# Kernel optimization log

Measured on AMD Instinct MI355X. Metric: run time of the kernel, lower is better.

The kernel has to match this reference:

```python
import jax, jax.numpy as jnp
import numpy as np

P_DROP = 0.2  # matches nn.Dropout(0.2) in the module __init__ (forward's dropout_p arg is unused)
DROPOUT_KEY = jax.random.key(42)  # deterministic dropout mask for reproducible baseline


def setup_inputs() -> dict:
    key = jax.random.key(0)
    kq, kk, kv = jax.random.split(key, 3)
    B, Sq, Sk, D, Dv = 4, 4096, 4096, 64, 64
    return {
        "q": jax.random.normal(kq, (B, Sq, D), dtype=jnp.float32),
        "k": jax.random.normal(kk, (B, Sk, D), dtype=jnp.float32),
        "v": jax.random.normal(kv, (B, Sk, Dv), dtype=jnp.float32),
        "scale_factor": 1,
        "dropout_p": 0,
    }


def reference(q, k, v, scale_factor, dropout_p):
    # qk = q @ k^T, scaled  -> [B, Sq, Sk] (full attention matrix, as in the original)
    qk = jnp.einsum("bqd,bkd->bqk", q, k) * scale_factor
    probs = jax.nn.softmax(qk, axis=-1)
    # dropout (train-mode nn.Dropout(p=0.2)): deterministic mask, inverted scaling
    keep = jax.random.bernoulli(DROPOUT_KEY, 1.0 - P_DROP, probs.shape)
    probs = jnp.where(keep, probs / (1.0 - P_DROP), 0.0)
    # output = probs @ v -> [B, Sq, Dv]
    return jnp.einsum("bqk,bkd->bqd", probs, v)
```

## Files before the change

kernel.cpp:

```cpp
#include <hip/hip_runtime.h>
#include <hip/hip_bf16.h>
#include <stdint.h>

typedef __attribute__((ext_vector_type(8))) _Float16 f16x8;
typedef __attribute__((ext_vector_type(4))) float f32x4;

static constexpr int BATCH = 4;
static constexpr int SEQ = 4096;
static constexpr int DIM = 64;
static constexpr int QB = 128;
static constexpr int NQB = SEQ / QB;
static constexpr uint32_t KEEP_THRESH = 0xCCCCCE00u;
static constexpr float LOG2E = 1.44269504088896340736f;

static constexpr size_t PB_BYTES = (QB * 64 + QB * 2) * 4;
static __host__ __device__ constexpr size_t ws_need(int ns) {
  return (size_t)BATCH * NQB * ns * PB_BYTES;
}
static __host__ __device__ constexpr size_t onum_bytes(int ns) {
  return (size_t)BATCH * NQB * ns * QB * 64 * 4;
}

__device__ __forceinline__ int lds_swz(int row, int colbyte) {
  return row * 128 + (colbyte ^ ((row & 7) << 4));
}

#define ROTL(x, r) (__builtin_amdgcn_alignbit((x), (x), 32 - (r)))

__device__ __forceinline__ bool tf_keep(uint32_t j42) {
  const uint32_t k1 = 42u;
  const uint32_t k2 = 0x1BD11BDAu ^ k1;
  uint32_t x1 = j42;
  uint32_t x0 = x1;
  x1 = ROTL(x1, 13) ^ x0;
  x0 += x1; x1 = ROTL(x1, 15) ^ x0;
  x0 += x1; x1 = ROTL(x1, 26) ^ x0;
  x0 += x1; x1 = ROTL(x1, 6)  ^ x0;
  x0 += k1;      x1 += k2 + 1u;
  x0 += x1; x1 = ROTL(x1, 17) ^ x0;
  x0 += x1; x1 = ROTL(x1, 29) ^ x0;
  x0 += x1; x1 = ROTL(x1, 16) ^ x0;
  x0 += x1; x1 = ROTL(x1, 24) ^ x0;
  x0 += k2;      x1 += 2u;
  x0 += x1; x1 = ROTL(x1, 13) ^ x0;
  x0 += x1; x1 = ROTL(x1, 15) ^ x0;
  x0 += x1; x1 = ROTL(x1, 26) ^ x0;
  x0 += x1; x1 = ROTL(x1, 6)  ^ x0;
    x1 += k1 + 3u;
  x0 += x1; x1 = ROTL(x1, 17) ^ x0;
  x0 += x1; x1 = ROTL(x1, 29) ^ x0;
  x0 += x1; x1 = ROTL(x1, 16) ^ x0;
  x0 += x1; x1 = ROTL(x1, 24) ^ x0;
  x0 += k1;      x1 += k2 + 4u;
  x0 += x1; x1 = ROTL(x1, 13) ^ x0;
  x0 += x1; x1 = ROTL(x1, 15) ^ x0;
  x0 += x1; x1 = ROTL(x1, 26) ^ x0;
  x0 += x1; x1 = ROTL(x1, 6)  ^ x0;
  x0 += k2;      x1 += 5u;
  return (x0 ^ x1) < KEEP_THRESH;
}

__device__ __forceinline__ float fexp2(float x) {
  float r;
  asm("v_exp_f32 %0, %1" : "=v"(r) : "v"(x));
  return r;
}

template<int CTRL>
__device__ __forceinline__ float dpp_movf(float x) {
  return __int_as_float(
      __builtin_amdgcn_mov_dpp(__float_as_int(x), CTRL, 0xF, 0xF, true));
}
__device__ __forceinline__ float red16_max(float v) {
  v = fmaxf(v, dpp_movf<0xB1>(v));
  v = fmaxf(v, dpp_movf<0x4E>(v));
  v = fmaxf(v, dpp_movf<0x141>(v));
  v = fmaxf(v, dpp_movf<0x140>(v));
  return v;
}
__device__ __forceinline__ float red16_add(float v) {
  v += dpp_movf<0xB1>(v);
  v += dpp_movf<0x4E>(v);
  v += dpp_movf<0x141>(v);
  v += dpp_movf<0x140>(v);
  return v;
}

template<bool PARTIAL, int NS>
__global__ __launch_bounds__(256, 3) void attn_kernel(
    const float* __restrict__ Q, const float* __restrict__ K, const float* __restrict__ V,
    const uint32_t* __restrict__ scale_raw,
    float* __restrict__ Out, float* __restrict__ onum, float* __restrict__ ml)
{
  __shared__ __align__(16) _Float16 Kld[64 * 64];
  __shared__ __align__(16) _Float16 Vt[64 * 64];
  __shared__ __align__(16) _Float16 Pld[4][32 * 64];

  const int b   = blockIdx.y;
  const int q0  = blockIdx.x * QB;
  const int tid = threadIdx.x;
  const int w    = tid >> 6;
  const int lane = tid & 63;
  const int l15  = lane & 15;
  const int l4   = lane >> 4;

  float scale;
  {
    uint32_t sb = *scale_raw;
    int e = (int)((sb >> 23) & 0xFFu);
    if (sb == 0u) scale = 0.0f;
    else if (e == 0 || e == 255) scale = (float)(int)sb;
    else scale = __uint_as_float(sb);
  }
  const float qscale = scale * LOG2E;

  const int qw = q0 + w * 32;

  uint32_t rcb42[2][4];
#pragma unroll
  for (int m = 0; m < 2; ++m)
#pragma unroll
    for (int r = 0; r < 4; ++r)
      rcb42[m][r] = ((uint32_t)(b * SEQ + qw + 16 * m + 4 * l4 + r)) * (uint32_t)SEQ + 42u;

  f16x8 aq[2][2];
#pragma unroll
  for (int m = 0; m < 2; ++m)
#pragma unroll
    for (int c = 0; c < 2; ++c) {
      const float* qp = Q + ((size_t)(b * SEQ + qw + 16 * m + l15)) * DIM + l4 * 8 + 32 * c;
      f16x8 h;
#pragma unroll
      for (int j = 0; j < 8; ++j) h[j] = (_Float16)(qp[j] * qscale);
      aq[m][c] = h;
    }

  float m_r[2][4], l_p[2][4];
  f32x4 Oacc[2][4];
#pragma unroll
  for (int m = 0; m < 2; ++m)
#pragma unroll
    for (int r = 0; r < 4; ++r) { m_r[m][r] = -INFINITY; l_p[m][r] = 0.0f; }
#pragma unroll
  for (int m = 0; m < 2; ++m)
#pragma unroll
    for (int n = 0; n < 4; ++n) Oacc[m][n] = f32x4{0.f, 0.f, 0.f, 0.f};

  const int nt = PARTIAL ? (SEQ / 64) / NS : SEQ / 64;
  const int t0 = PARTIAL ? (int)blockIdx.z * nt : 0;

  const int kr  = tid >> 4;
  const int kd0 = (tid & 15) * 4;
  const int vd  = tid & 63;
  const int vq  = tid >> 6;

  for (int kt = 0; kt < nt; ++kt) {
    const int kbase = (t0 + kt) * 64;
    __syncthreads();
#pragma unroll
    for (int i = 0; i < 4; ++i) {
      int k = kr + 16 * i;
      float4 kf = *(const float4*)(K + ((size_t)(b * SEQ + kbase + k)) * DIM + kd0);
      _Float16 h0 = (_Float16)kf.x, h1 = (_Float16)kf.y,
               h2 = (_Float16)kf.z, h3 = (_Float16)kf.w;
      *(ushort4*)((char*)Kld + lds_swz(k, kd0 * 2)) = ushort4{
        __builtin_bit_cast(unsigned short, h0), __builtin_bit_cast(unsigned short, h1),
        __builtin_bit_cast(unsigned short, h2), __builtin_bit_cast(unsigned short, h3)};
    }
#pragma unroll
    for (int i = 0; i < 4; ++i) {
      int k0 = vq * 4 + 16 * i;
      const float* vp = V + ((size_t)(b * SEQ + kbase + k0)) * DIM + vd;
      float v0 = vp[0], v1 = vp[DIM], v2 = vp[2 * DIM], v3 = vp[3 * DIM];
      unsigned int p01 = __builtin_bit_cast(unsigned int, __builtin_amdgcn_cvt_pkrtz(v0, v1));
      unsigned int p23 = __builtin_bit_cast(unsigned int, __builtin_amdgcn_cvt_pkrtz(v2, v3));
      *(uint2*)((char*)Vt + lds_swz(vd, k0 * 2)) = uint2{p01, p23};
    }
    __syncthreads();

    char* pw = (char*)&Pld[w][0];

#pragma unroll
    for (int m = 0; m < 2; ++m) {
      f32x4 s[4];
#pragma unroll
      for (int n = 0; n < 4; ++n) {
        f32x4 acc = f32x4{0.f, 0.f, 0.f, 0.f};
#pragma unroll
        for (int c = 0; c < 2; ++c) {
          int off = lds_swz(16 * n + l15, (l4 * 8 + 32 * c) * 2);
          f16x8 bk = *(const f16x8*)((char*)Kld + off);
          acc = __builtin_amdgcn_mfma_f32_16x16x32_f16(aq[m][c], bk, acc, 0, 0, 0);
        }
        s[n] = acc;
      }

      float mnew[4];
#pragma unroll
      for (int r = 0; r < 4; ++r)
        mnew[r] = red16_max(fmaxf(fmaxf(s[0][r], s[1][r]), fmaxf(s[2][r], s[3][r])));

#pragma unroll
      for (int r = 0; r < 4; ++r) {
        float mn = fmaxf(m_r[m][r], mnew[r]);
        float corr = fexp2(m_r[m][r] - mn);
        m_r[m][r] = mn;
        l_p[m][r] *= corr;
#pragma unroll
        for (int n = 0; n < 4; ++n) Oacc[m][n][r] *= corr;
      }

#pragma unroll
      for (int n = 0; n < 4; ++n) {
        uint32_t cb = (uint32_t)(kbase + l15 + 16 * n);
#pragma unroll
        for (int r = 0; r < 4; ++r) {
          float e = fexp2(s[n][r] - m_r[m][r]);
          l_p[m][r] += e;
          float p = tf_keep(rcb42[m][r] + cb) ? e : 0.0f;
          *(_Float16*)(pw + lds_swz(16 * m + 4 * l4 + r, (l15 + 16 * n) * 2)) = (_Float16)p;
        }
      }
    }

    asm volatile("s_waitcnt lgkmcnt(0)" ::: "memory");
    __builtin_amdgcn_sched_barrier(0);

    f16x8 pa[2][2];
#pragma unroll
    for (int m = 0; m < 2; ++m)
#pragma unroll
      for (int c = 0; c < 2; ++c)
        pa[m][c] = *(const f16x8*)(pw + lds_swz(16 * m + l15, (l4 * 8 + 32 * c) * 2));
#pragma unroll
    for (int n = 0; n < 4; ++n) {
#pragma unroll
      for (int c = 0; c < 2; ++c) {
        f16x8 bv = *(const f16x8*)((char*)Vt + lds_swz(l15 + 16 * n, (l4 * 8 + 32 * c) * 2));
#pragma unroll
        for (int m = 0; m < 2; ++m)
          Oacc[m][n] = __builtin_amdgcn_mfma_f32_16x16x32_f16(pa[m][c], bv, Oacc[m][n], 0, 0, 0);
      }
    }
  }

  if (PARTIAL) {
    const int pb = ((b * NQB + (int)blockIdx.x) * NS + (int)blockIdx.z);
    float* op = onum + (size_t)pb * (QB * 64);
#pragma unroll
    for (int m = 0; m < 2; ++m)
#pragma unroll
      for (int r = 0; r < 4; ++r) {
        int row = w * 32 + 16 * m + 4 * l4 + r;
        float lr = red16_add(l_p[m][r]);
#pragma unroll
        for (int n = 0; n < 4; ++n)
          op[row * 64 + l15 + 16 * n] = Oacc[m][n][r];
        if (l15 == 0) {
          ml[(size_t)pb * (QB * 2) + row * 2 + 0] = m_r[m][r];
          ml[(size_t)pb * (QB * 2) + row * 2 + 1] = lr;
        }
      }
  } else {
#pragma unroll
    for (int m = 0; m < 2; ++m)
#pragma unroll
      for (int r = 0; r < 4; ++r) {
        float L = red16_add(l_p[m][r]);
        float inv = 1.0f / (L * 0.8f);
        int qg = qw + 16 * m + 4 * l4 + r;
        float* op = Out + ((size_t)(b * SEQ + qg)) * DIM + l15;
#pragma unroll
        for (int n = 0; n < 4; ++n)
          op[16 * n] = Oacc[m][n][r] * inv;
      }
  }
}

template<int NS>
__global__ __launch_bounds__(256) void combine_kernel(
    const float* __restrict__ onum, const float* __restrict__ ml, float* __restrict__ Out)
{
  const int w = threadIdx.x >> 6;
  const int lane = threadIdx.x & 63;
  const int rid = blockIdx.x * 4 + w;
  const int b = rid >> 12;
  const int qrow = rid & 4095;
  const int qb = qrow >> 7;
  const int r128 = qrow & 127;
  const int pb0 = (b * NQB + qb) * NS;

  float m[NS], l[NS];
  float M = -INFINITY;
#pragma unroll
  for (int s = 0; s < NS; ++s) {
    m[s] = ml[(size_t)(pb0 + s) * (QB * 2) + r128 * 2 + 0];
    l[s] = ml[(size_t)(pb0 + s) * (QB * 2) + r128 * 2 + 1];
    M = fmaxf(M, m[s]);
  }
  float L = 0.0f, acc = 0.0f;
#pragma unroll
  for (int s = 0; s < NS; ++s) {
    float sc = fexp2(m[s] - M);
    L += l[s] * sc;
    acc += onum[(size_t)(pb0 + s) * (QB * 64) + r128 * 64 + lane] * sc;
  }
  Out[(size_t)rid * 64 + lane] = acc / (L * 0.8f);
}

extern "C" void kernel_launch(void* const* d_in, const int* in_sizes, int n_in,
                              void* d_out, int out_size, void* d_ws, size_t ws_size,
                              hipStream_t stream) {
  const float* Q = (const float*)d_in[0];
  const float* K = (const float*)d_in[1];
  const float* V = (const float*)d_in[2];
  const uint32_t* scale_raw = (const uint32_t*)d_in[3];
  float* Out = (float*)d_out;

  if (ws_size >= ws_need(8)) {
    float* onum = (float*)d_ws;
    float* ml = (float*)((char*)d_ws + onum_bytes(8));
    attn_kernel<true, 8><<<dim3(NQB, BATCH, 8), 256, 0, stream>>>(
        Q, K, V, scale_raw, nullptr, onum, ml);
    combine_kernel<8><<<SEQ * BATCH / 4, 256, 0, stream>>>(onum, ml, Out);
  } else if (ws_size >= ws_need(4)) {
    float* onum = (float*)d_ws;
    float* ml = (float*)((char*)d_ws + onum_bytes(4));
    attn_kernel<true, 4><<<dim3(NQB, BATCH, 4), 256, 0, stream>>>(
        Q, K, V, scale_raw, nullptr, onum, ml);
    combine_kernel<4><<<SEQ * BATCH / 4, 256, 0, stream>>>(onum, ml, Out);
  } else {
    attn_kernel<false, 1><<<dim3(NQB, BATCH, 1), 256, 0, stream>>>(
        Q, K, V, scale_raw, Out, nullptr, nullptr);
  }
}
```

Baseline: 172.3 us.

## Shrink query block to 64 rows with one 16-row MFMA tile per wave

Halves the query block from 128 to 64 rows so each wave handles 16 query rows instead of 32, removing the inner m loop and cutting per-wave register state. This doubles the grid size, which improves parallelism and load balance. In exchange, K/V tiles are loaded and converted twice as often per query row, roughly doubling global-to-LDS traffic, and launch bounds occupancy hint drops from 3 to 2.

```diff
diff --git a/kernel.cpp b/kernel.cpp
--- a/kernel.cpp
+++ b/kernel.cpp
@@ -8,7 +8,7 @@
 static constexpr int BATCH = 4;
 static constexpr int SEQ = 4096;
 static constexpr int DIM = 64;
-static constexpr int QB = 128;
+static constexpr int QB = 64;
 static constexpr int NQB = SEQ / QB;
 static constexpr uint32_t KEEP_THRESH = 0xCCCCCE00u;
 static constexpr float LOG2E = 1.44269504088896340736f;
@@ -87,14 +87,14 @@
 }
 
 template<bool PARTIAL, int NS>
-__global__ __launch_bounds__(256, 3) void attn_kernel(
+__global__ __launch_bounds__(256, 2) void attn_kernel(
     const float* __restrict__ Q, const float* __restrict__ K, const float* __restrict__ V,
     const uint32_t* __restrict__ scale_raw,
     float* __restrict__ Out, float* __restrict__ onum, float* __restrict__ ml)
 {
   __shared__ __align__(16) _Float16 Kld[64 * 64];
   __shared__ __align__(16) _Float16 Vt[64 * 64];
-  __shared__ __align__(16) _Float16 Pld[4][32 * 64];
+  __shared__ __align__(16) _Float16 Pld[4][16 * 64];
 
   const int b   = blockIdx.y;
   const int q0  = blockIdx.x * QB;
@@ -114,37 +114,29 @@
   }
   const float qscale = scale * LOG2E;
 
-  const int qw = q0 + w * 32;
-
-  uint32_t rcb42[2][4];
-#pragma unroll
-  for (int m = 0; m < 2; ++m)
-#pragma unroll
-    for (int r = 0; r < 4; ++r)
-      rcb42[m][r] = ((uint32_t)(b * SEQ + qw + 16 * m + 4 * l4 + r)) * (uint32_t)SEQ + 42u;
-
-  f16x8 aq[2][2];
-#pragma unroll
-  for (int m = 0; m < 2; ++m)
-#pragma unroll
-    for (int c = 0; c < 2; ++c) {
-      const float* qp = Q + ((size_t)(b * SEQ + qw + 16 * m + l15)) * DIM + l4 * 8 + 32 * c;
-      f16x8 h;
-#pragma unroll
-      for (int j = 0; j < 8; ++j) h[j] = (_Float16)(qp[j] * qscale);
-      aq[m][c] = h;
-    }
-
-  float m_r[2][4], l_p[2][4];
-  f32x4 Oacc[2][4];
-#pragma unroll
-  for (int m = 0; m < 2; ++m)
-#pragma unroll
-    for (int r = 0; r < 4; ++r) { m_r[m][r] = -INFINITY; l_p[m][r] = 0.0f; }
-#pragma unroll
-  for (int m = 0; m < 2; ++m)
-#pragma unroll
-    for (int n = 0; n < 4; ++n) Oacc[m][n] = f32x4{0.f, 0.f, 0.f, 0.f};
+  const int qw = q0 + w * 16;
+
+  uint32_t rcb42[4];
+#pragma unroll
+  for (int r = 0; r < 4; ++r)
+    rcb42[r] = ((uint32_t)(b * SEQ + qw + 4 * l4 + r)) * (uint32_t)SEQ + 42u;
+
+  f16x8 aq[2];
+#pragma unroll
+  for (int c = 0; c < 2; ++c) {
+    const float* qp = Q + ((size_t)(b * SEQ + qw + l15)) * DIM + l4 * 8 + 32 * c;
+    f16x8 h;
+#pragma unroll
+    for (int j = 0; j < 8; ++j) h[j] = (_Float16)(qp[j] * qscale);
+    aq[c] = h;
+  }
+
+  float m_r[4], l_p[4];
+  f32x4 Oacc[4];
+#pragma unroll
+  for (int r = 0; r < 4; ++r) { m_r[r] = -INFINITY; l_p[r] = 0.0f; }
+#pragma unroll
+  for (int n = 0; n < 4; ++n) Oacc[n] = f32x4{0.f, 0.f, 0.f, 0.f};
 
   const int nt = PARTIAL ? (SEQ / 64) / NS : SEQ / 64;
   const int t0 = PARTIAL ? (int)blockIdx.z * nt : 0;
@@ -178,68 +170,60 @@
     }
     __syncthreads();
 
+    f32x4 s[4];
+#pragma unroll
+    for (int n = 0; n < 4; ++n) {
+      f32x4 acc = f32x4{0.f, 0.f, 0.f, 0.f};
+#pragma unroll
+      for (int c = 0; c < 2; ++c) {
+        int off = lds_swz(16 * n + l15, (l4 * 8 + 32 * c) * 2);
+        f16x8 bk = *(const f16x8*)((char*)Kld + off);
+        acc = __builtin_amdgcn_mfma_f32_16x16x32_f16(aq[c], bk, acc, 0, 0, 0);
+      }
+      s[n] = acc;
+    }
+
+    float mnew[4];
+#pragma unroll
+    for (int r = 0; r < 4; ++r)
+      mnew[r] = red16_max(fmaxf(fmaxf(s[0][r], s[1][r]), fmaxf(s[2][r], s[3][r])));
+
+#pragma unroll
+    for (int r = 0; r < 4; ++r) {
+      float mn = fmaxf(m_r[r], mnew[r]);
+      float corr = fexp2(m_r[r] - mn);
+      m_r[r] = mn;
+      l_p[r] *= corr;
+#pragma unroll
+      for (int n = 0; n < 4; ++n) Oacc[n][r] *= corr;
+    }
+
     char* pw = (char*)&Pld[w][0];
-
-#pragma unroll
-    for (int m = 0; m < 2; ++m) {
-      f32x4 s[4];
-#pragma unroll
-      for (int n = 0; n < 4; ++n) {
-        f32x4 acc = f32x4{0.f, 0.f, 0.f, 0.f};
-#pragma unroll
-        for (int c = 0; c < 2; ++c) {
-          int off = lds_swz(16 * n + l15, (l4 * 8 + 32 * c) * 2);
-          f16x8 bk = *(const f16x8*)((char*)Kld + off);
-          acc = __builtin_amdgcn_mfma_f32_16x16x32_f16(aq[m][c], bk, acc, 0, 0, 0);
-        }
-        s[n] = acc;
-      }
-
-      float mnew[4];
-#pragma unroll
-      for (int r = 0; r < 4; ++r)
-        mnew[r] = red16_max(fmaxf(fmaxf(s[0][r], s[1][r]), fmaxf(s[2][r], s[3][r])));
-
+#pragma unroll
+    for (int n = 0; n < 4; ++n) {
+      uint32_t cb = (uint32_t)(kbase + l15 + 16 * n);
 #pragma unroll
       for (int r = 0; r < 4; ++r) {
-        float mn = fmaxf(m_r[m][r], mnew[r]);
-        float corr = fexp2(m_r[m][r] - mn);
-        m_r[m][r] = mn;
-        l_p[m][r] *= corr;
-#pragma unroll
-        for (int n = 0; n < 4; ++n) Oacc[m][n][r] *= corr;
-      }
-
-#pragma unroll
-      for (int n = 0; n < 4; ++n) {
-        uint32_t cb = (uint32_t)(kbase + l15 + 16 * n);
-#pragma unroll
-        for (int r = 0; r < 4; ++r) {
-          float e = fexp2(s[n][r] - m_r[m][r]);
-          l_p[m][r] += e;
-          float p = tf_keep(rcb42[m][r] + cb) ? e : 0.0f;
-          *(_Float16*)(pw + lds_swz(16 * m + 4 * l4 + r, (l15 + 16 * n) * 2)) = (_Float16)p;
-        }
+        float e = fexp2(s[n][r] - m_r[r]);
+        l_p[r] += e;
+        float p = tf_keep(rcb42[r] + cb) ? e : 0.0f;
+        *(_Float16*)(pw + lds_swz(4 * l4 + r, (l15 + 16 * n) * 2)) = (_Float16)p;
       }
     }
 
     asm volatile("s_waitcnt lgkmcnt(0)" ::: "memory");
     __builtin_amdgcn_sched_barrier(0);
 
-    f16x8 pa[2][2];
-#pragma unroll
-    for (int m = 0; m < 2; ++m)
-#pragma unroll
-      for (int c = 0; c < 2; ++c)
-        pa[m][c] = *(const f16x8*)(pw + lds_swz(16 * m + l15, (l4 * 8 + 32 * c) * 2));
+    f16x8 pa[2];
+#pragma unroll
+    for (int c = 0; c < 2; ++c)
+      pa[c] = *(const f16x8*)(pw + lds_swz(l15, (l4 * 8 + 32 * c) * 2));
 #pragma unroll
     for (int n = 0; n < 4; ++n) {
 #pragma unroll
       for (int c = 0; c < 2; ++c) {
         f16x8 bv = *(const f16x8*)((char*)Vt + lds_swz(l15 + 16 * n, (l4 * 8 + 32 * c) * 2));
-#pragma unroll
-        for (int m = 0; m < 2; ++m)
-          Oacc[m][n] = __builtin_amdgcn_mfma_f32_16x16x32_f16(pa[m][c], bv, Oacc[m][n], 0, 0, 0);
+        Oacc[n] = __builtin_amdgcn_mfma_f32_16x16x32_f16(pa[c], bv, Oacc[n], 0, 0, 0);
       }
     }
   }
@@ -248,32 +232,28 @@
     const int pb = ((b * NQB + (int)blockIdx.x) * NS + (int)blockIdx.z);
     float* op = onum + (size_t)pb * (QB * 64);
 #pragma unroll
-    for (int m = 0; m < 2; ++m)
-#pragma unroll
-      for (int r = 0; r < 4; ++r) {
-        int row = w * 32 + 16 * m + 4 * l4 + r;
-        float lr = red16_add(l_p[m][r]);
-#pragma unroll
-        for (int n = 0; n < 4; ++n)
-          op[row * 64 + l15 + 16 * n] = Oacc[m][n][r];
-        if (l15 == 0) {
-          ml[(size_t)pb * (QB * 2) + row * 2 + 0] = m_r[m][r];
-          ml[(size_t)pb * (QB * 2) + row * 2 + 1] = lr;
-        }
+    for (int r = 0; r < 4; ++r) {
+      int row = w * 16 + 4 * l4 + r;
+      float lr = red16_add(l_p[r]);
+#pragma unroll
+      for (int n = 0; n < 4; ++n)
+        op[row * 64 + l15 + 16 * n] = Oacc[n][r];
+      if (l15 == 0) {
+        ml[(size_t)pb * (QB * 2) + row * 2 + 0] = m_r[r];
+        ml[(size_t)pb * (QB * 2) + row * 2 + 1] = lr;
       }
+    }
   } else {
 #pragma unroll
-    for (int m = 0; m < 2; ++m)
-#pragma unroll
-      for (int r = 0; r < 4; ++r) {
-        float L = red16_add(l_p[m][r]);
-        float inv = 1.0f / (L * 0.8f);
-        int qg = qw + 16 * m + 4 * l4 + r;
-        float* op = Out + ((size_t)(b * SEQ + qg)) * DIM + l15;
-#pragma unroll
-        for (int n = 0; n < 4; ++n)
-          op[16 * n] = Oacc[m][n][r] * inv;
-      }
+    for (int r = 0; r < 4; ++r) {
+      float L = red16_add(l_p[r]);
+      float inv = 1.0f / (L * 0.8f);
+      int qg = qw + 4 * l4 + r;
+      float* op = Out + ((size_t)(b * SEQ + qg)) * DIM + l15;
+#pragma unroll
+      for (int n = 0; n < 4; ++n)
+        op[16 * n] = Oacc[n][r] * inv;
+    }
   }
 }
 
@@ -286,16 +266,16 @@
   const int rid = blockIdx.x * 4 + w;
   const int b = rid >> 12;
   const int qrow = rid & 4095;
-  const int qb = qrow >> 7;
-  const int r128 = qrow & 127;
+  const int qb = qrow >> 6;
+  const int r64 = qrow & 63;
   const int pb0 = (b * NQB + qb) * NS;
 
   float m[NS], l[NS];
   float M = -INFINITY;
 #pragma unroll
   for (int s = 0; s < NS; ++s) {
-    m[s] = ml[(size_t)(pb0 + s) * (QB * 2) + r128 * 2 + 0];
-    l[s] = ml[(size_t)(pb0 + s) * (QB * 2) + r128 * 2 + 1];
+    m[s] = ml[(size_t)(pb0 + s) * (QB * 2) + r64 * 2 + 0];
+    l[s] = ml[(size_t)(pb0 + s) * (QB * 2) + r64 * 2 + 1];
     M = fmaxf(M, m[s]);
   }
   float L = 0.0f, acc = 0.0f;
@@ -303,7 +283,7 @@
   for (int s = 0; s < NS; ++s) {
     float sc = fexp2(m[s] - M);
     L += l[s] * sc;
-    acc += onum[(size_t)(pb0 + s) * (QB * 64) + r128 * 64 + lane] * sc;
+    acc += onum[(size_t)(pb0 + s) * (QB * 64) + r64 * 64 + lane] * sc;
   }
   Out[(size_t)rid * 64 + lane] = acc / (L * 0.8f);
 }
```

New measurement: 178.4 us. +3.5%, slower.
